# Kernel tuning notes

Hardware: AMD Instinct MI355X
Metric: run time of the kernel (lower is better)

## Reference

```python
import jax, jax.numpy as jnp
import numpy as np

N_NODES = 50000

def setup_inputs() -> dict:
    key = jax.random.key(0)
    k1, k2, k3, k4, k5 = jax.random.split(key, 5)
    x = jax.random.normal(k1, (50000, 512), dtype=jnp.float32)
    edge_row = jax.random.randint(k2, (800000,), 0, N_NODES, dtype=jnp.int64)
    edge_col = jax.random.randint(k3, (800000,), 0, N_NODES, dtype=jnp.int64)
    edge_val = jax.random.uniform(k4, (800000,), dtype=jnp.float32)
    # init like torch: uniform(-stdv, stdv), stdv = 1/sqrt(out_features)
    stdv = 1.0 / np.sqrt(96.0)
    weight = jax.random.uniform(k5, (512, 96), minval=-stdv, maxval=stdv, dtype=jnp.float32)
    return {"x": x, "edge_row": edge_row, "edge_col": edge_col, "edge_val": edge_val, "weight": weight}

def reference(x, edge_row, edge_col, edge_val, weight):
    # support = X @ W  -- dense GEMM [N, F_in] x [F_in, F_out]
    support = x @ weight
    # sparse adjacency matmul: out[row] += val * support[col]
    msgs = edge_val[:, None] * support[edge_col]          # [E, F_out]
    out = jax.ops.segment_sum(msgs, edge_row, num_segments=N_NODES)
    # act = ReLU (module default); bias=False
    return jax.nn.relu(out)
```

## Files before the change

kernel.cpp:

```cpp
#include <hip/hip_runtime.h>

#define N_NODES 50000
#define F_IN    512
#define F_OUT   96
#define N_EDGES 800000

#define RPB    128
#define NBKT   391
#define CAP    2560
#define ECHUNK 4096
#define NCHUNK ((N_EDGES + ECHUNK - 1) / ECHUNK)
#define GEMM_BLOCKS ((N_NODES + 63) / 64)

typedef __attribute__((ext_vector_type(8))) short bf16x8;
typedef __attribute__((ext_vector_type(4))) float f32x4;

typedef const __attribute__((address_space(1))) void* gas_ptr;
typedef __attribute__((address_space(3))) void* las_ptr;

__device__ __forceinline__ void gload_lds16(const void* g, void* l) {
    __builtin_amdgcn_global_load_lds((gas_ptr)g, (las_ptr)l, 16, 0, 0);
}

__device__ __forceinline__ unsigned short f2bf(float f) {
    unsigned int u = __float_as_uint(f);
    unsigned int r = (u + 0x7FFFu + ((u >> 16) & 1u)) >> 16;
    return (unsigned short)r;
}
__device__ __forceinline__ float bf2f(unsigned short h) {
    return __uint_as_float(((unsigned int)h) << 16);
}

__global__ __launch_bounds__(256) void k_wcast(const float* __restrict__ w,
                                               unsigned short* __restrict__ wTp,
                                               int* __restrict__ bcnt) {
    if (blockIdx.x == 0) {
        const int t = threadIdx.x;
        bcnt[t] = 0;
        if (t < 144) bcnt[256 + t] = 0;
    }
    const int i = blockIdx.x * 256 + threadIdx.x;
    if (i < F_OUT * F_IN) {
        const int n  = i >> 9;
        const int k  = i & 511;
        const int p  = k >> 6;
        const int kk = k & 63;
        const int slot = kk ^ ((n & 7) << 3);
        wTp[p * (F_OUT * 64) + n * 64 + slot] = f2bf(w[(size_t)k * F_OUT + n]);
    }
}

__global__ __launch_bounds__(256) void k_fused(const float* __restrict__ x,
                                               const unsigned short* __restrict__ wTp,
                                               unsigned short* __restrict__ support,
                                               const int* __restrict__ erow,
                                               const int* __restrict__ ecol,
                                               const float* __restrict__ eval,
                                               int* __restrict__ bcnt,
                                               float2* __restrict__ bucket) {
    __shared__ __align__(16) char smem[40960];
    const int tid = threadIdx.x;

    if (blockIdx.x < NCHUNK) {
        int* hist  = (int*)smem;
        int* gbase = hist + 400;
        int* lcur  = gbase + 400;
        for (int i = tid; i < NBKT; i += 256) { hist[i] = 0; lcur[i] = 0; }
        __syncthreads();

        const int base = blockIdx.x * ECHUNK;
        const int n = min(ECHUNK, N_EDGES - base);

        for (int i = tid; i < n; i += 256)
            atomicAdd(&hist[erow[base + i] >> 7], 1);
        __syncthreads();

        for (int b = tid; b < NBKT; b += 256)
            gbase[b] = hist[b] ? atomicAdd(&bcnt[b], hist[b]) : 0;
        __syncthreads();

        for (int i = tid; i < n; i += 256) {
            const int r = erow[base + i];
            const int b = r >> 7;
            const int pos = gbase[b] + atomicAdd(&lcur[b], 1);
            if (pos >= 0 && pos < CAP)
                bucket[(size_t)b * CAP + pos] = make_float2(
                    __int_as_float(((r & 127) << 16) | ecol[base + i]),
                    eval[base + i]);
        }
        return;
    }

    unsigned short (*sX)[64 * 64] = (unsigned short (*)[64 * 64])smem;
    unsigned short (*sB)[64 * 96] = (unsigned short (*)[64 * 96])(smem + 16384);

    const int lane = tid & 63;
    const int wave = tid >> 6;
    const int r0   = (blockIdx.x - NCHUNK) * 64;
    const int lr   = lane & 15;
    const int kg   = lane >> 4;

    f32x4 acc[6];
    #pragma unroll
    for (int t = 0; t < 6; ++t) acc[t] = (f32x4){0.f, 0.f, 0.f, 0.f};

    float4 xr[4];

    auto XLOAD = [&](int p) {
        #pragma unroll
        for (int i = 0; i < 4; ++i) {
            const int chunk = i * 256 + tid;
            const int row   = chunk >> 4;
            const int c     = chunk & 15;
            int gr = r0 + row;
            if (gr > N_NODES - 1) gr = N_NODES - 1;
            xr[i] = *reinterpret_cast<const float4*>(x + (size_t)gr * F_IN + p * 64 + c * 4);
        }
    };
    auto XWRITE = [&](int buf) {
        char* xb = (char*)&sX[buf][0];
        #pragma unroll
        for (int i = 0; i < 4; ++i) {
            const int chunk = i * 256 + tid;
            const int row   = chunk >> 4;
            const int c     = chunk & 15;
            ushort4 h;
            h.x = f2bf(xr[i].x); h.y = f2bf(xr[i].y);
            h.z = f2bf(xr[i].z); h.w = f2bf(xr[i].w);
            const int byte = (c * 8) ^ ((row & 7) << 4);
            *reinterpret_cast<ushort4*>(xb + row * 128 + byte) = h;
        }
    };
    auto BSTAGE = [&](int buf, int p) {
        #pragma unroll
        for (int i = 0; i < 3; ++i) {
            const int chunk = i * 256 + tid;
            gload_lds16(wTp + (size_t)p * (F_OUT * 64) + chunk * 8,
                        &sB[buf][chunk * 8]);
        }
    };
    auto COMPUTE = [&](int buf) {
        const char* xb = (const char*)&sX[buf][0];
        const char* bb = (const char*)&sB[buf][0];
        const int xrow = wave * 16 + lr;
        #pragma unroll
        for (int ks = 0; ks < 2; ++ks) {
            const int off = (ks * 64 + kg * 16) ^ ((xrow & 7) << 4);
            const bf16x8 af = *reinterpret_cast<const bf16x8*>(xb + xrow * 128 + off);
            #pragma unroll
            for (int t = 0; t < 6; ++t) {
                const int n    = t * 16 + lr;
                const int boff = (ks * 64 + kg * 16) ^ ((n & 7) << 4);
                const bf16x8 bfr = *reinterpret_cast<const bf16x8*>(bb + n * 128 + boff);
                acc[t] = __builtin_amdgcn_mfma_f32_16x16x32_bf16(af, bfr, acc[t], 0, 0, 0);
            }
        }
    };

    XLOAD(0);
    BSTAGE(0, 0);
    XWRITE(0);
    __syncthreads();
    for (int t = 0; t < 8; ++t) {
        if (t < 7) { XLOAD(t + 1); BSTAGE((t + 1) & 1, t + 1); }
        COMPUTE(t & 1);
        if (t < 7) XWRITE((t + 1) & 1);
        __syncthreads();
    }

    #pragma unroll
    for (int t = 0; t < 6; ++t) {
        #pragma unroll
        for (int r = 0; r < 4; ++r) {
            const int row = r0 + wave * 16 + kg * 4 + r;
            if (row < N_NODES)
                support[(size_t)row * F_OUT + t * 16 + lr] = f2bf(acc[t][r]);
        }
    }
}

__global__ __launch_bounds__(256) void kS_sort(const int* __restrict__ bcnt,
                                               const float2* __restrict__ bucket,
                                               float2* __restrict__ bucket2,
                                               int* __restrict__ rowOffs) {
    __shared__ int cnt[RPB];
    __shared__ int sc[RPB];
    __shared__ int rbase[RPB];
    __shared__ int rcur[RPB];
    const int b   = blockIdx.x;
    const int tid = threadIdx.x;

    if (tid < RPB) { cnt[tid] = 0; rcur[tid] = 0; }
    __syncthreads();

    const int beg = b * CAP;
    const int n   = min(bcnt[b], CAP);

    for (int i = tid; i < n; i += 256)
        atomicAdd(&cnt[(__float_as_int(bucket[beg + i].x) >> 16) & 127], 1);
    __syncthreads();

    if (tid < RPB) sc[tid] = cnt[tid];
    __syncthreads();
    #pragma unroll
    for (int off = 1; off < RPB; off <<= 1) {
        int a = 0;
        if (tid < RPB && tid >= off) a = sc[tid - off];
        __syncthreads();
        if (tid < RPB) sc[tid] += a;
        __syncthreads();
    }
    if (tid < RPB) {
        const int rb = beg + sc[tid] - cnt[tid];
        rbase[tid] = rb;
        rowOffs[b * 129 + tid] = rb;
    }
    if (tid == RPB) rowOffs[b * 129 + RPB] = beg + n;
    __syncthreads();

    for (int i = tid; i < n; i += 256) {
        const float2 ev  = bucket[beg + i];
        const int    key = __float_as_int(ev.x);
        const int    r   = (key >> 16) & 127;
        const int    pos = rbase[r] + atomicAdd(&rcur[r], 1);
        bucket2[pos] = make_float2(__int_as_float(key & 0xFFFF), ev.y);
    }
}

__global__ __launch_bounds__(256) void k_gather(const int* __restrict__ rowOffs,
                                                const float2* __restrict__ bucket2,
                                                const unsigned short* __restrict__ support,
                                                float* __restrict__ out) {
    const int gid = blockIdx.x * 256 + threadIdx.x;
    if (gid >= N_NODES * 6) return;
    const int r   = gid / 6;
    const int f16 = gid - r * 6;

    const int idx = (r >> 7) * 129 + (r & 127);
    const int beg = rowOffs[idx];
    const int end = rowOffs[idx + 1];

    float acc[16];
    #pragma unroll
    for (int j = 0; j < 16; ++j) acc[j] = 0.f;

    for (int i = beg; i < end; ++i) {
        const float2 cv = bucket2[i];
        const int   c = __float_as_int(cv.x);
        const float v = cv.y;
        const unsigned short* sp = support + (size_t)c * F_OUT + f16 * 16;
        const bf16x8 s0 = *reinterpret_cast<const bf16x8*>(sp);
        const bf16x8 s1 = *reinterpret_cast<const bf16x8*>(sp + 8);
        #pragma unroll
        for (int j = 0; j < 8; ++j) {
            acc[j]     = fmaf(v, bf2f((unsigned short)s0[j]), acc[j]);
            acc[8 + j] = fmaf(v, bf2f((unsigned short)s1[j]), acc[8 + j]);
        }
    }

    float* o = out + (size_t)r * F_OUT + f16 * 16;
    #pragma unroll
    for (int q = 0; q < 4; ++q) {
        float4 ov;
        ov.x = fmaxf(acc[q * 4 + 0], 0.f);
        ov.y = fmaxf(acc[q * 4 + 1], 0.f);
        ov.z = fmaxf(acc[q * 4 + 2], 0.f);
        ov.w = fmaxf(acc[q * 4 + 3], 0.f);
        *reinterpret_cast<float4*>(o + q * 4) = ov;
    }
}

extern "C" void kernel_launch(void* const* d_in, const int* in_sizes, int n_in,
                              void* d_out, int out_size, void* d_ws, size_t ws_size,
                              hipStream_t stream) {
    const float* x    = (const float*)d_in[0];
    const int*   erow = (const int*)d_in[1];
    const int*   ecol = (const int*)d_in[2];
    const float* eval = (const float*)d_in[3];
    const float* w    = (const float*)d_in[4];
    float*       out  = (float*)d_out;

    unsigned short* support = (unsigned short*)d_ws;
    int*    bcnt    = (int*)((char*)d_ws + 9600000);
    int*    rowOffs = bcnt + 400;
    unsigned short* wTp = (unsigned short*)(rowOffs + 50560);
    float2* bucket  = (float2*)((char*)wTp + 98304);
    float2* bucket2 = bucket + (size_t)NBKT * CAP;

    k_wcast<<<(F_OUT * F_IN + 255) / 256, 256, 0, stream>>>(w, wTp, bcnt);

    k_fused<<<NCHUNK + GEMM_BLOCKS, 256, 0, stream>>>(x, wTp, support,
                                                      erow, ecol, eval,
                                                      bcnt, bucket);

    kS_sort<<<NBKT, 256, 0, stream>>>(bcnt, bucket, bucket2, rowOffs);

    const int gthreads = N_NODES * 6;
    k_gather<<<(gthreads + 255) / 256, 256, 0, stream>>>(rowOffs, bucket2, support, out);
}
```

Measured before the change: 81.96 us.

## Load X fragments directly into registers and stage W in two halves

The GEMM part of the fused kernel stops staging X through LDS. Each lane now loads its own MFMA A-fragment straight from global memory into registers, with a software prefetch a few k-steps ahead, and converts to bf16 just before the MFMA. The weight is staged into a larger LDS buffer in two halves of four k-panels each, which replaces the per-step double buffer and cuts the barriers to a handful. This removes the LDS write/read round trip for X and most of the per-iteration syncs, at the cost of more registers (up to 32 float4 per thread) and fewer, larger LDS stalls while W is staged.

```diff
diff --git a/kernel.cpp b/kernel.cpp
--- a/kernel.cpp
+++ b/kernel.cpp
@@ -58,7 +58,7 @@
                                                const float* __restrict__ eval,
                                                int* __restrict__ bcnt,
                                                float2* __restrict__ bucket) {
-    __shared__ __align__(16) char smem[40960];
+    __shared__ __align__(16) char smem[49152];
     const int tid = threadIdx.x;
 
     if (blockIdx.x < NCHUNK) {
@@ -91,8 +91,7 @@
         return;
     }
 
-    unsigned short (*sX)[64 * 64] = (unsigned short (*)[64 * 64])smem;
-    unsigned short (*sB)[64 * 96] = (unsigned short (*)[64 * 96])(smem + 16384);
+    unsigned short* sB = (unsigned short*)smem;
 
     const int lane = tid & 63;
     const int wave = tid >> 6;
@@ -100,53 +99,42 @@
     const int lr   = lane & 15;
     const int kg   = lane >> 4;
 
+    int grow = r0 + wave * 16 + lr;
+    if (grow > N_NODES - 1) grow = N_NODES - 1;
+    const float* xrow = x + (size_t)grow * F_IN + kg * 8;
+
     f32x4 acc[6];
     #pragma unroll
     for (int t = 0; t < 6; ++t) acc[t] = (f32x4){0.f, 0.f, 0.f, 0.f};
 
-    float4 xr[4];
-
+    float4 ar[8][4];
+
+    auto BSTAGE = [&](int half) {
+        const unsigned short* src = wTp + (size_t)half * (4 * F_OUT * 64);
+        #pragma unroll
+        for (int i = 0; i < 12; ++i) {
+            const int chunk = i * 256 + tid;
+            gload_lds16(src + chunk * 8, sB + chunk * 8);
+        }
+    };
     auto XLOAD = [&](int p) {
-        #pragma unroll
-        for (int i = 0; i < 4; ++i) {
-            const int chunk = i * 256 + tid;
-            const int row   = chunk >> 4;
-            const int c     = chunk & 15;
-            int gr = r0 + row;
-            if (gr > N_NODES - 1) gr = N_NODES - 1;
-            xr[i] = *reinterpret_cast<const float4*>(x + (size_t)gr * F_IN + p * 64 + c * 4);
-        }
+        const float* b = xrow + p * 64;
+        ar[p][0] = *reinterpret_cast<const float4*>(b);
+        ar[p][1] = *reinterpret_cast<const float4*>(b + 4);
+        ar[p][2] = *reinterpret_cast<const float4*>(b + 32);
+        ar[p][3] = *reinterpret_cast<const float4*>(b + 36);
     };
-    auto XWRITE = [&](int buf) {
-        char* xb = (char*)&sX[buf][0];
-        #pragma unroll
-        for (int i = 0; i < 4; ++i) {
-            const int chunk = i * 256 + tid;
-            const int row   = chunk >> 4;
-            const int c     = chunk & 15;
-            ushort4 h;
-            h.x = f2bf(xr[i].x); h.y = f2bf(xr[i].y);
-            h.z = f2bf(xr[i].z); h.w = f2bf(xr[i].w);
-            const int byte = (c * 8) ^ ((row & 7) << 4);
-            *reinterpret_cast<ushort4*>(xb + row * 128 + byte) = h;
-        }
-    };
-    auto BSTAGE = [&](int buf, int p) {
-        #pragma unroll
-        for (int i = 0; i < 3; ++i) {
-            const int chunk = i * 256 + tid;
-            gload_lds16(wTp + (size_t)p * (F_OUT * 64) + chunk * 8,
-                        &sB[buf][chunk * 8]);
-        }
-    };
-    auto COMPUTE = [&](int buf) {
-        const char* xb = (const char*)&sX[buf][0];
-        const char* bb = (const char*)&sB[buf][0];
-        const int xrow = wave * 16 + lr;
+    auto COMPUTE = [&](int p) {
+        const char* bb = (const char*)(sB + (p & 3) * (F_OUT * 64));
         #pragma unroll
         for (int ks = 0; ks < 2; ++ks) {
-            const int off = (ks * 64 + kg * 16) ^ ((xrow & 7) << 4);
-            const bf16x8 af = *reinterpret_cast<const bf16x8*>(xb + xrow * 128 + off);
+            const float4 a0 = ar[p][ks * 2];
+            const float4 a1 = ar[p][ks * 2 + 1];
+            bf16x8 af;
+            af[0] = (short)f2bf(a0.x); af[1] = (short)f2bf(a0.y);
+            af[2] = (short)f2bf(a0.z); af[3] = (short)f2bf(a0.w);
+            af[4] = (short)f2bf(a1.x); af[5] = (short)f2bf(a1.y);
+            af[6] = (short)f2bf(a1.z); af[7] = (short)f2bf(a1.w);
             #pragma unroll
             for (int t = 0; t < 6; ++t) {
                 const int n    = t * 16 + lr;
@@ -157,16 +145,21 @@
         }
     };
 
-    XLOAD(0);
-    BSTAGE(0, 0);
-    XWRITE(0);
-    __syncthreads();
-    for (int t = 0; t < 8; ++t) {
-        if (t < 7) { XLOAD(t + 1); BSTAGE((t + 1) & 1, t + 1); }
-        COMPUTE(t & 1);
-        if (t < 7) XWRITE((t + 1) & 1);
-        __syncthreads();
-    }
+    BSTAGE(0);
+    __syncthreads();
+    XLOAD(0); XLOAD(1); XLOAD(2);
+    COMPUTE(0); XLOAD(3);
+    COMPUTE(1); XLOAD(4);
+    COMPUTE(2); XLOAD(5);
+    COMPUTE(3);
+    __syncthreads();
+    BSTAGE(1);
+    __syncthreads();
+    XLOAD(6);
+    COMPUTE(4); XLOAD(7);
+    COMPUTE(5);
+    COMPUTE(6);
+    COMPUTE(7);
 
     #pragma unroll
     for (int t = 0; t < 6; ++t) {
```

New measurement: 83.72 us. 1.02x slower.

## Pre-pack weights in MFMA fragment order and load B directly from global

Applied to the files above, without the earlier changes.

The weight-cast kernel now writes the bf16 weight in per-lane MFMA fragment order, so each lane can load its B operand with a single contiguous 16-byte global read. The GEMM no longer stages W through LDS with global_load_lds, which shrinks shared memory from 40 KB to 16 KB and may allow more resident blocks. The cost is that every wave re-reads its B fragments from global/L2 on each k-step rather than sharing one LDS copy.

```diff
diff --git a/kernel.cpp b/kernel.cpp
--- a/kernel.cpp
+++ b/kernel.cpp
@@ -15,13 +15,6 @@
 typedef __attribute__((ext_vector_type(8))) short bf16x8;
 typedef __attribute__((ext_vector_type(4))) float f32x4;
 
-typedef const __attribute__((address_space(1))) void* gas_ptr;
-typedef __attribute__((address_space(3))) void* las_ptr;
-
-__device__ __forceinline__ void gload_lds16(const void* g, void* l) {
-    __builtin_amdgcn_global_load_lds((gas_ptr)g, (las_ptr)l, 16, 0, 0);
-}
-
 __device__ __forceinline__ unsigned short f2bf(float f) {
     unsigned int u = __float_as_uint(f);
     unsigned int r = (u + 0x7FFFu + ((u >> 16) & 1u)) >> 16;
@@ -32,7 +25,7 @@
 }
 
 __global__ __launch_bounds__(256) void k_wcast(const float* __restrict__ w,
-                                               unsigned short* __restrict__ wTp,
+                                               unsigned short* __restrict__ wTq,
                                                int* __restrict__ bcnt) {
     if (blockIdx.x == 0) {
         const int t = threadIdx.x;
@@ -41,24 +34,29 @@
     }
     const int i = blockIdx.x * 256 + threadIdx.x;
     if (i < F_OUT * F_IN) {
-        const int n  = i >> 9;
-        const int k  = i & 511;
-        const int p  = k >> 6;
-        const int kk = k & 63;
-        const int slot = kk ^ ((n & 7) << 3);
-        wTp[p * (F_OUT * 64) + n * 64 + slot] = f2bf(w[(size_t)k * F_OUT + n]);
+        const int j    = i & 7;
+        const int lane = (i >> 3) & 63;
+        const int ks   = (i >> 9) & 1;
+        const int tp   = i >> 10;
+        const int t    = tp % 6;
+        const int p    = tp / 6;
+        const int lr   = lane & 15;
+        const int kg   = lane >> 4;
+        const int n    = t * 16 + lr;
+        const int k    = p * 64 + ks * 32 + kg * 8 + j;
+        wTq[i] = f2bf(w[(size_t)k * F_OUT + n]);
     }
 }
 
 __global__ __launch_bounds__(256) void k_fused(const float* __restrict__ x,
-                                               const unsigned short* __restrict__ wTp,
+                                               const unsigned short* __restrict__ wTq,
                                                unsigned short* __restrict__ support,
                                                const int* __restrict__ erow,
                                                const int* __restrict__ ecol,
                                                const float* __restrict__ eval,
                                                int* __restrict__ bcnt,
                                                float2* __restrict__ bucket) {
-    __shared__ __align__(16) char smem[40960];
+    __shared__ __align__(16) char smem[16384];
     const int tid = threadIdx.x;
 
     if (blockIdx.x < NCHUNK) {
@@ -92,7 +90,6 @@
     }
 
     unsigned short (*sX)[64 * 64] = (unsigned short (*)[64 * 64])smem;
-    unsigned short (*sB)[64 * 96] = (unsigned short (*)[64 * 96])(smem + 16384);
 
     const int lane = tid & 63;
     const int wave = tid >> 6;
@@ -131,40 +128,30 @@
             *reinterpret_cast<ushort4*>(xb + row * 128 + byte) = h;
         }
     };
-    auto BSTAGE = [&](int buf, int p) {
-        #pragma unroll
-        for (int i = 0; i < 3; ++i) {
-            const int chunk = i * 256 + tid;
-            gload_lds16(wTp + (size_t)p * (F_OUT * 64) + chunk * 8,
-                        &sB[buf][chunk * 8]);
-        }
-    };
-    auto COMPUTE = [&](int buf) {
+    auto COMPUTE = [&](int buf, int p) {
         const char* xb = (const char*)&sX[buf][0];
-        const char* bb = (const char*)&sB[buf][0];
         const int xrow = wave * 16 + lr;
+        const unsigned short* bbase = wTq + ((size_t)p * 12) * 512 + lane * 8;
         #pragma unroll
         for (int ks = 0; ks < 2; ++ks) {
             const int off = (ks * 64 + kg * 16) ^ ((xrow & 7) << 4);
             const bf16x8 af = *reinterpret_cast<const bf16x8*>(xb + xrow * 128 + off);
             #pragma unroll
             for (int t = 0; t < 6; ++t) {
-                const int n    = t * 16 + lr;
-                const int boff = (ks * 64 + kg * 16) ^ ((n & 7) << 4);
-                const bf16x8 bfr = *reinterpret_cast<const bf16x8*>(bb + n * 128 + boff);
-                acc[t] = __builtin_amdgcn_mfma_f32_16x16x32_bf16(af, bfr, acc[t], 0, 0, 0);
+                const bf16x8 bq = *reinterpret_cast<const bf16x8*>(
+                    bbase + (t * 2 + ks) * 512);
+                acc[t] = __builtin_amdgcn_mfma_f32_16x16x32_bf16(af, bq, acc[t], 0, 0, 0);
             }
         }
     };
 
     XLOAD(0);
-    BSTAGE(0, 0);
     XWRITE(0);
     __syncthreads();
-    for (int t = 0; t < 8; ++t) {
-        if (t < 7) { XLOAD(t + 1); BSTAGE((t + 1) & 1, t + 1); }
-        COMPUTE(t & 1);
-        if (t < 7) XWRITE((t + 1) & 1);
+    for (int p = 0; p < 8; ++p) {
+        if (p < 7) XLOAD(p + 1);
+        COMPUTE(p & 1, p);
+        if (p < 7) XWRITE((p + 1) & 1);
         __syncthreads();
     }
 
@@ -283,13 +270,13 @@
     unsigned short* support = (unsigned short*)d_ws;
     int*    bcnt    = (int*)((char*)d_ws + 9600000);
     int*    rowOffs = bcnt + 400;
-    unsigned short* wTp = (unsigned short*)(rowOffs + 50560);
-    float2* bucket  = (float2*)((char*)wTp + 98304);
+    unsigned short* wTq = (unsigned short*)(rowOffs + 50560);
+    float2* bucket  = (float2*)((char*)wTq + 98304);
     float2* bucket2 = bucket + (size_t)NBKT * CAP;
 
-    k_wcast<<<(F_OUT * F_IN + 255) / 256, 256, 0, stream>>>(w, wTp, bcnt);
-
-    k_fused<<<NCHUNK + GEMM_BLOCKS, 256, 0, stream>>>(x, wTp, support,
+    k_wcast<<<(F_OUT * F_IN + 255) / 256, 256, 0, stream>>>(w, wTq, bcnt);
+
+    k_fused<<<NCHUNK + GEMM_BLOCKS, 256, 0, stream>>>(x, wTq, support,
                                                       erow, ecol, eval,
                                                       bcnt, bucket);
 
```

Result: no change. 82.21 us (+0.3%).
